# Performance work log

Hardware: AMD Instinct MI355X
Metric: run time of the kernel (lower is better)

Reference implementation:

```python
import jax, jax.numpy as jnp
import numpy as np

EPS = 1e-5
GROUPS = 32


def conv2d(x, w, b):
    # x: [N,C,H,W], w: [O,I,3,3] (or 1x1), stride 1, padding 'same' for 3x3
    kh = w.shape[2]
    pad = (kh - 1) // 2
    y = jax.lax.conv_general_dilated(x, w, (1, 1), ((pad, pad), (pad, pad)),
                                     dimension_numbers=('NCHW', 'OIHW', 'NCHW'))
    return y + b[None, :, None, None]


def group_norm(x, g, b):
    N, C, H, W = x.shape
    xr = x.reshape(N, GROUPS, C // GROUPS, H, W)
    mu = xr.mean(axis=(2, 3, 4), keepdims=True)
    var = xr.var(axis=(2, 3, 4), keepdims=True)
    xr = (xr - mu) / jnp.sqrt(var + EPS)
    return xr.reshape(N, C, H, W) * g[None, :, None, None] + b[None, :, None, None]


def batch_norm(x, g, b):
    # training-mode BatchNorm2d: batch statistics over (N,H,W)
    mu = x.mean(axis=(0, 2, 3), keepdims=True)
    var = x.var(axis=(0, 2, 3), keepdims=True)
    return (x - mu) / jnp.sqrt(var + EPS) * g[None, :, None, None] + b[None, :, None, None]


def binary_activation(x):
    # STE: forward sign(x), backward through piecewise poly out3
    out_fwd = jnp.sign(x)
    m1 = (x < -1).astype(x.dtype)
    m2 = (x < 0).astype(x.dtype)
    m3 = (x < 1).astype(x.dtype)
    out1 = -1.0 * m1 + (x * x + 2.0 * x) * (1.0 - m1)
    out2 = out1 * m2 + (-x * x + 2.0 * x) * (1.0 - m2)
    out3 = out2 * m3 + 1.0 * (1.0 - m3)
    return jax.lax.stop_gradient(out_fwd - out3) + out3


def hard_binary_conv(x, w, b):
    # per-output-channel scaling * sign(w), STE through clipped weights
    scale = jax.lax.stop_gradient(jnp.mean(jnp.abs(w), axis=(1, 2, 3), keepdims=True))
    bw_ng = scale * jnp.sign(w)
    clipped = jnp.clip(w, -1.0, 1.0)
    bw = jax.lax.stop_gradient(bw_ng - clipped) + clipped
    return conv2d(x, bw, b)


def learnable_bias(x, emb, w, b):
    bias = jax.nn.silu(emb) @ w.T + b  # [B, C]
    return x + bias[:, :, None, None]


def _forward(c, x, emb,
             rb_gn1_g, rb_gn1_b, rb_conv1_w, rb_conv1_b, rb_emb_w, rb_emb_b,
             rb_gn2_g, rb_gn2_b, rb_conv2_w, rb_conv2_b,
             m1_w, m1_b, bconv_w, bconv_b, bn_g, bn_b,
             m2_w, m2_b, prelu_a, m3_w, m3_b):
    # ResBlock (skip = Identity since out_channels == channels)
    h = conv2d(jax.nn.silu(group_norm(c, rb_gn1_g, rb_gn1_b)), rb_conv1_w, rb_conv1_b)
    eo = jax.nn.silu(emb) @ rb_emb_w.T + rb_emb_b          # [B, 2*C]
    scale, shift = jnp.split(eo[:, :, None, None], 2, axis=1)
    h = group_norm(h, rb_gn2_g, rb_gn2_b) * (1.0 + scale) + shift
    h = conv2d(jax.nn.silu(h), rb_conv2_w, rb_conv2_b)
    c2 = c + h
    # concat + bias + STE binarize + binary conv + BN + channel-pool residual + PReLU
    xc = jnp.concatenate([x, c2], axis=1)                   # [B, 2C, H, W]
    out = learnable_bias(xc, emb, m1_w, m1_b)
    out = binary_activation(out)
    out = hard_binary_conv(out, bconv_w, bconv_b)
    out = batch_norm(out, bn_g, bn_b)
    N, C2, H, W = xc.shape
    out = out + xc.reshape(N, C2 // 2, 2, H, W).mean(axis=2)  # channel mean pooling
    out = learnable_bias(out, emb, m2_w, m2_b)
    out = jnp.where(out >= 0, out, prelu_a[None, :, None, None] * out)  # PReLU
    out = learnable_bias(out, emb, m3_w, m3_b)
    return out


def setup_inputs() -> dict:
    key = jax.random.key(0)
    ks = jax.random.split(key, 24)
    B, C, EMB, H, W = 8, 128, 512, 64, 64
    IN2 = 2 * C
    n = lambda k, s, sc=0.05: jax.random.normal(k, s, dtype=jnp.float32) * sc
    return {
        'c': jax.random.normal(ks[0], (B, C, H, W), dtype=jnp.float32),
        'x': jax.random.normal(ks[1], (B, C, H, W), dtype=jnp.float32),
        'emb': jax.random.normal(ks[2], (B, EMB), dtype=jnp.float32),
        'rb_gn1_g': jnp.ones((C,), jnp.float32), 'rb_gn1_b': jnp.zeros((C,), jnp.float32),
        'rb_conv1_w': n(ks[3], (C, C, 3, 3)), 'rb_conv1_b': n(ks[4], (C,)),
        'rb_emb_w': n(ks[5], (2 * C, EMB)), 'rb_emb_b': n(ks[6], (2 * C,)),
        'rb_gn2_g': jnp.ones((C,), jnp.float32), 'rb_gn2_b': jnp.zeros((C,), jnp.float32),
        'rb_conv2_w': n(ks[7], (C, C, 3, 3)), 'rb_conv2_b': n(ks[8], (C,)),
        'm1_w': n(ks[9], (IN2, EMB)), 'm1_b': n(ks[10], (IN2,)),
        'bconv_w': jax.random.uniform(ks[11], (C, IN2, 3, 3), dtype=jnp.float32) * 0.001,
        'bconv_b': n(ks[12], (C,)),
        'bn_g': jnp.ones((C,), jnp.float32), 'bn_b': jnp.zeros((C,), jnp.float32),
        'm2_w': n(ks[13], (C, EMB)), 'm2_b': n(ks[14], (C,)),
        'prelu_a': jnp.full((C,), 0.25, jnp.float32),
        'm3_w': n(ks[15], (C, EMB)), 'm3_b': n(ks[16], (C,)),
    }


def reference(c, x, emb,
              rb_gn1_g, rb_gn1_b, rb_conv1_w, rb_conv1_b, rb_emb_w, rb_emb_b,
              rb_gn2_g, rb_gn2_b, rb_conv2_w, rb_conv2_b,
              m1_w, m1_b, bconv_w, bconv_b, bn_g, bn_b,
              m2_w, m2_b, prelu_a, m3_w, m3_b):
    return _forward(c, x, emb,
                    rb_gn1_g, rb_gn1_b, rb_conv1_w, rb_conv1_b, rb_emb_w, rb_emb_b,
                    rb_gn2_g, rb_gn2_b, rb_conv2_w, rb_conv2_b,
                    m1_w, m1_b, bconv_w, bconv_b, bn_g, bn_b,
                    m2_w, m2_b, prelu_a, m3_w, m3_b)
```

## Files before the change

### kernel.cpp

```cpp
#include <hip/hip_runtime.h>
#include <stdint.h>


#define B_   8
#define C_   128
#define C2_  256
#define HW_  4096
#define EMB_ 512
#define EPS_ 1e-5f

typedef int   v16i __attribute__((ext_vector_type(16)));
typedef float v16f __attribute__((ext_vector_type(16)));
typedef short v8s  __attribute__((ext_vector_type(8)));
typedef int   v4i  __attribute__((ext_vector_type(4)));

#define COLB 272
#define ROWB (66 * COLB)
#define LDSZ 55296
#define TSTRIDE 132

__device__ __forceinline__ float silu(float v) {
    return v * __builtin_amdgcn_rcpf(1.f + __expf(-v));
}
__device__ __forceinline__ unsigned short f2bf(float f) {
    unsigned int x = __float_as_uint(f);
    return (unsigned short)((x + 0x7FFFu + ((x >> 16) & 1u)) >> 16);
}
__device__ __forceinline__ int8_t sgn8(float v) {
    return (v > 0.f) ? (int8_t)1 : ((v < 0.f) ? (int8_t)(-1) : (int8_t)0);
}
__device__ __forceinline__ void gld16(char* ldst, const char* gsrc) {
    __builtin_amdgcn_global_load_lds((const unsigned int*)gsrc,
                                     (unsigned int*)ldst, 16, 0, 0);
}

__global__ __launch_bounds__(256) void k_prep(
    const float* __restrict__ w, int8_t* __restrict__ sgn,
    float* __restrict__ alpha, float* __restrict__ bnPS, float* __restrict__ bnPQ,
    float* __restrict__ gnS, float* __restrict__ gnQ,
    const float* __restrict__ w1, const float* __restrict__ w2,
    unsigned short* __restrict__ Wc1, unsigned short* __restrict__ Wc2,
    const float* __restrict__ emb,
    const float* __restrict__ ew, const float* __restrict__ ebb,
    const float* __restrict__ m1w, const float* __restrict__ m1b,
    const float* __restrict__ m2w, const float* __restrict__ m2b,
    const float* __restrict__ m3w, const float* __restrict__ m3b,
    float* __restrict__ eo, float* __restrict__ b1,
    float* __restrict__ b2, float* __restrict__ b3,
    const float* __restrict__ gin,
    float* __restrict__ g1S, float* __restrict__ g1Q,
    int8_t* __restrict__ S) {
    __shared__ float red[256];
    const int blk = blockIdx.x, tid = threadIdx.x;
    if (blk < 128) {
        const int o = blk;
        if (o == 0) {
            for (int i = tid; i < 1024; i += 256) { bnPS[i] = 0.f; bnPQ[i] = 0.f; }
        }
        if (o == 1) { gnS[tid] = 0.f; }
        if (o == 2) { gnQ[tid] = 0.f; }
        const float* wr = w + (size_t)o * (C2_ * 9);
        float s = 0.f;
        for (int i = tid; i < C2_ * 9; i += 256) s += fabsf(wr[i]);
        red[tid] = s;
        __syncthreads();
        for (int st = 128; st > 0; st >>= 1) {
            if (tid < st) red[tid] += red[tid + st];
            __syncthreads();
        }
        if (tid == 0) alpha[o] = red[0] / (float)(C2_ * 9);
        for (int kk = 0; kk < 9; ++kk) {
            float v = wr[tid * 9 + kk];
            sgn[((size_t)(kk * 16 + (tid >> 4)) * C_ + o) * 16 + (tid & 15)] = sgn8(v);
        }
    } else if (blk < 704) {
        int i = (blk - 128) * 256 + tid;
        int co = i / (C_ * 9);
        int rem = i - co * (C_ * 9);
        int ci = rem / 9, kk = rem - ci * 9;
        size_t d = ((size_t)(kk * 16 + (ci >> 3)) * C_ + co) * 8 + (ci & 7);
        Wc1[d] = f2bf(w1[i]);
        Wc2[d] = f2bf(w2[i]);
    } else if (blk < 896) {
        const int o = (blk - 704) * 4 + (tid >> 6);
        const int l = tid & 63;
        const float* wv;
        float bias;
        float* dst;
        int dstride;
        if (o < 256)      { wv = ew  + (size_t)o * EMB_;              bias = ebb[o];    dst = eo + o;  dstride = 256; }
        else if (o < 512) { int r = o - 256; wv = m1w + (size_t)r * EMB_; bias = m1b[r]; dst = b1 + r; dstride = 256; }
        else if (o < 640) { int r = o - 512; wv = m2w + (size_t)r * EMB_; bias = m2b[r]; dst = b2 + r; dstride = 128; }
        else              { int r = o - 640; wv = m3w + (size_t)r * EMB_; bias = m3b[r]; dst = b3 + r; dstride = 128; }
        const float4 wa = *(const float4*)(wv + 8 * l);
        const float4 wb = *(const float4*)(wv + 8 * l + 4);
#pragma unroll
        for (int b = 0; b < B_; ++b) {
            const float* s = emb + b * EMB_ + 8 * l;
            float4 sa = *(const float4*)(s);
            float4 sb = *(const float4*)(s + 4);
            float p = wa.x * silu(sa.x) + wa.y * silu(sa.y) + wa.z * silu(sa.z) + wa.w * silu(sa.w) +
                      wb.x * silu(sb.x) + wb.y * silu(sb.y) + wb.z * silu(sb.z) + wb.w * silu(sb.w);
#pragma unroll
            for (int off = 32; off > 0; off >>= 1) p += __shfl_down(p, off, 64);
            if (l == 0) dst[b * dstride] = bias + p;
        }
    } else if (blk < 1408) {
        const int idx = blk - 896;
        const int n = idx >> 6, rest = idx & 63, grp = rest >> 1, h = rest & 1;
        const size_t base = ((size_t)(n * C_ + grp * 4)) << 12;
        float sum = 0.f, sq = 0.f;
        const float4* in4 = (const float4*)(gin + base);
        for (int i = tid + h * 2048; i < (h + 1) * 2048; i += 256) {
            float4 v = in4[i];
            sum += v.x + v.y + v.z + v.w;
            sq += v.x * v.x + v.y * v.y + v.z * v.z + v.w * v.w;
        }
#pragma unroll
        for (int off = 32; off > 0; off >>= 1) {
            sum += __shfl_xor(sum, off, 64);
            sq  += __shfl_xor(sq, off, 64);
        }
        if ((tid & 63) == 0) { red[tid >> 6] = sum; red[8 + (tid >> 6)] = sq; }
        __syncthreads();
        if (tid == 0) {
            g1S[h * 256 + n * 32 + grp] = red[0] + red[1] + red[2] + red[3];
            g1Q[h * 256 + n * 32 + grp] = red[8] + red[9] + red[10] + red[11];
        }
    } else {
        const int u = blk - 1408;
        const int n = u >> 1;
        const int row = (u & 1) * 65;
        int4* base = (int4*)(S + (size_t)n * 66 * ROWB + (size_t)row * ROWB);
        const int4 z = make_int4(0, 0, 0, 0);
        for (int i = tid; i < ROWB / 16; i += 256) base[i] = z;
    }
}

__global__ __launch_bounds__(512, 4) void k_conv1(
    const float* __restrict__ cin,
    const unsigned short* __restrict__ Wc,
    const float* __restrict__ bias,
    const float* __restrict__ g1w, const float* __restrict__ g1b,
    const float* __restrict__ g1S, const float* __restrict__ g1Q,
    float* __restrict__ outN,
    float* __restrict__ gnS, float* __restrict__ gnQ) {
    __shared__ __align__(16) char lds[LDSZ];
    __shared__ float chA[128], chB[128];
    const int y = blockIdx.x;
    const int n = blockIdx.y;
    const int tid = threadIdx.x;

    if (tid < 128) {
        const int ch = tid, grp = tid >> 2;
        const float s1 = g1S[n * 32 + grp] + g1S[256 + n * 32 + grp];
        const float q1 = g1Q[n * 32 + grp] + g1Q[256 + n * 32 + grp];
        const float mu = s1 * (1.f / 16384.f);
        const float var = q1 * (1.f / 16384.f) - mu * mu;
        const float rstd = rsqrtf(var + EPS_);
        const float A = g1w[ch] * rstd;
        chA[ch] = A;
        chB[ch] = g1b[ch] - mu * A;
    }
    if (tid < 96) {
        int r = tid / 32, q = tid & 31;
        int c = (q >> 4) ? 65 : 0, o = q & 15;
        *(float4*)(lds + (r * 66 + c) * COLB + o * 16) = make_float4(0.f, 0.f, 0.f, 0.f);
    }
    __syncthreads();

    union F4 { float4 v; float f[4]; };
#pragma unroll
    for (int u = 0; u < 6; ++u) {
        int unit = u * 512 + tid;
        int r = unit >> 10, rem = unit & 1023;
        int cp = rem >> 4, s4 = rem & 15;
        int ch0 = 2 * cp;
        int yy = y - 1 + r;
        char* dst0 = lds + (r * 66 + 4 * s4 + 1) * COLB + 4 * cp;
        if (yy >= 0 && yy < 64) {
            const float* src = cin + (((size_t)(n * C_ + ch0)) << 12) + yy * 64 + 4 * s4;
            F4 fa, fb;
            fa.v = *(const float4*)src;
            fb.v = *(const float4*)(src + HW_);
            const float A0 = chA[ch0], B0 = chB[ch0];
            const float A1 = chA[ch0 + 1], B1 = chB[ch0 + 1];
#pragma unroll
            for (int e = 0; e < 4; ++e) {
                unsigned int lo = f2bf(silu(fa.f[e] * A0 + B0));
                unsigned int hi = f2bf(silu(fb.f[e] * A1 + B1));
                *(unsigned int*)(dst0 + e * COLB) = lo | (hi << 16);
            }
        } else {
#pragma unroll
            for (int e = 0; e < 4; ++e)
                *(unsigned int*)(dst0 + e * COLB) = 0u;
        }
    }
    __syncthreads();

    const int w = tid >> 6;
    const int og = w >> 1;
    const int ph = w & 1;
    const int l = tid & 63;
    const int lm = l & 31;
    const int lh = l >> 5;

    v16f acc;
#pragma unroll
    for (int i = 0; i < 16; ++i) acc[i] = 0.f;

#pragma unroll
    for (int kk = 0; kk < 9; ++kk) {
        const int r = kk / 3, dx = kk % 3 - 1;
        const char* col = lds + (r * 66 + 32 * ph + lm + 1 + dx) * COLB + 16 * lh;
        const unsigned short* wbase = Wc + (size_t)(kk * 16 + lh) * C_ * 8 + (32 * og + lm) * 8;
#pragma unroll
        for (int cb = 0; cb < 8; ++cb) {
            v8s a = *(const v8s*)(wbase + (size_t)(2 * cb) * C_ * 8);
            v8s b = *(const v8s*)(col + 32 * cb);
            acc = __builtin_amdgcn_mfma_f32_32x32x16_bf16(a, b, acc, 0, 0, 0);
        }
    }
    __syncthreads();
    float* ldsT = (float*)lds;
    float* ldsS = (float*)(lds + 64 * TSTRIDE * 4);
    float* ldsQ = ldsS + 256;
#pragma unroll
    for (int r = 0; r < 16; ++r) {
        const int row = (r & 3) + 8 * (r >> 2) + 4 * lh;
        const int co = 32 * og + row;
        float v = acc[r] + bias[co];
        ldsT[(32 * ph + lm) * TSTRIDE + co] = v;
        float p = v, q = v * v;
#pragma unroll
        for (int m = 16; m > 0; m >>= 1) {
            p += __shfl_xor(p, m, 64);
            q += __shfl_xor(q, m, 64);
        }
        if (lm == 0) { ldsS[ph * 128 + co] = p; ldsQ[ph * 128 + co] = q; }
    }
    __syncthreads();
    if (tid < 32) {
        const int g = tid;
        float p = 0.f, q = 0.f;
#pragma unroll
        for (int j = 0; j < 4; ++j) {
            p += ldsS[4 * g + j] + ldsS[128 + 4 * g + j];
            q += ldsQ[4 * g + j] + ldsQ[128 + 4 * g + j];
        }
        atomicAdd(&gnS[n * 32 + g], p);
        atomicAdd(&gnQ[n * 32 + g], q);
    }
    const int q4 = tid & 31;
    float* orow = outN + (((size_t)(n * HW_) + (y << 6)) << 7);
#pragma unroll
    for (int it = 0; it < 4; ++it) {
        const int px = it * 16 + (tid >> 5);
        *(float4*)(orow + ((size_t)px << 7) + 4 * q4) =
            *(const float4*)(ldsT + px * TSTRIDE + 4 * q4);
    }
}

__global__ __launch_bounds__(512, 4) void k_conv2(
    const float* __restrict__ yin,
    const unsigned short* __restrict__ Wc,
    const float* __restrict__ bias,
    const float* __restrict__ res,
    const float* __restrict__ xin,
    const float* __restrict__ b1v,
    const float* __restrict__ eo,
    const float* __restrict__ g2,
    const float* __restrict__ bt2,
    const float* __restrict__ gnS,
    const float* __restrict__ gnQ,
    float* __restrict__ poolC2,
    int8_t* __restrict__ S) {
    __shared__ __align__(16) char lds[LDSZ];
    __shared__ float ldsA[128], ldsB[128];
    const int y = blockIdx.x;
    const int n = blockIdx.y;
    const int tid = threadIdx.x;

    if (tid < 128) {
        const int ch = tid, grp = tid >> 2;
        const float mu = gnS[n * 32 + grp] * (1.f / 16384.f);
        const float var = gnQ[n * 32 + grp] * (1.f / 16384.f) - mu * mu;
        const float rstd = rsqrtf(var + EPS_);
        const float gg = g2[ch] * rstd;
        const float sc = 1.f + eo[n * 256 + ch];
        ldsA[ch] = gg * sc;
        ldsB[ch] = (bt2[ch] - mu * gg) * sc + eo[n * 256 + 128 + ch];
    }
    if (tid < 96) {
        int r = tid / 32, q = tid & 31;
        int cpad = (q >> 4) ? 65 : 0, o = q & 15;
        *(float4*)(lds + (r * 66 + cpad) * COLB + o * 16) = make_float4(0.f, 0.f, 0.f, 0.f);
    }
    __syncthreads();

    const int qc = tid & 31;
    const float A0 = ldsA[4 * qc], A1 = ldsA[4 * qc + 1], A2 = ldsA[4 * qc + 2], A3 = ldsA[4 * qc + 3];
    const float B0 = ldsB[4 * qc], B1 = ldsB[4 * qc + 1], B2 = ldsB[4 * qc + 2], B3 = ldsB[4 * qc + 3];
#pragma unroll
    for (int r = 0; r < 3; ++r) {
        const int yy = y - 1 + r;
        const float* ysrc = yin + (((size_t)(n * HW_) + yy * 64) << 7);
        const bool ok = (yy >= 0 && yy < 64);
#pragma unroll
        for (int it = 0; it < 4; ++it) {
            const int px = it * 16 + (tid >> 5);
            char* dst = lds + (r * 66 + px + 1) * COLB + qc * 8;
            if (ok) {
                float4 v = *(const float4*)(ysrc + ((size_t)px << 7) + 4 * qc);
                union { unsigned short u[4]; uint2 q; } pk;
                pk.u[0] = f2bf(silu(v.x * A0 + B0));
                pk.u[1] = f2bf(silu(v.y * A1 + B1));
                pk.u[2] = f2bf(silu(v.z * A2 + B2));
                pk.u[3] = f2bf(silu(v.w * A3 + B3));
                *(uint2*)dst = pk.q;
            } else {
                *(uint2*)dst = make_uint2(0u, 0u);
            }
        }
    }
    __syncthreads();

    const int w = tid >> 6;
    const int og = w >> 1;
    const int ph = w & 1;
    const int l = tid & 63;
    const int lm = l & 31;
    const int lh = l >> 5;

    v16f acc;
#pragma unroll
    for (int i = 0; i < 16; ++i) acc[i] = 0.f;

#pragma unroll
    for (int kk = 0; kk < 9; ++kk) {
        const int r = kk / 3, dx = kk % 3 - 1;
        const char* col = lds + (r * 66 + 32 * ph + lm + 1 + dx) * COLB + 16 * lh;
        const unsigned short* wbase = Wc + (size_t)(kk * 16 + lh) * C_ * 8 + (32 * og + lm) * 8;
#pragma unroll
        for (int cb = 0; cb < 8; ++cb) {
            v8s a = *(const v8s*)(wbase + (size_t)(2 * cb) * C_ * 8);
            v8s b = *(const v8s*)(col + 32 * cb);
            acc = __builtin_amdgcn_mfma_f32_32x32x16_bf16(a, b, acc, 0, 0, 0);
        }
    }
    float c2v[16];
#pragma unroll
    for (int r = 0; r < 16; ++r) {
        const int row = (r & 3) + 8 * (r >> 2) + 4 * lh;
        const int co = 32 * og + row;
        const size_t o = (((size_t)n * C_ + co) << 12) + (y << 6);
        c2v[r] = acc[r] + bias[co] + res[o + 32 * ph + lm];
    }
#pragma unroll
    for (int q = 0; q < 4; ++q) {
        const int pc = 16 * og + 4 * q + 2 * lh;
        const size_t po = (((size_t)n * 64 + pc) << 12) + (y << 6);
        poolC2[po + 32 * ph + lm]        = 0.5f * (c2v[4 * q] + c2v[4 * q + 1]);
        poolC2[po + 4096 + 32 * ph + lm] = 0.5f * (c2v[4 * q + 2] + c2v[4 * q + 3]);
    }

    __syncthreads();
#pragma unroll
    for (int q = 0; q < 4; ++q) {
        const int co0 = 32 * og + 8 * q + 4 * lh;
        const float b0 = b1v[n * 256 + 128 + co0];
        const float b1b = b1v[n * 256 + 128 + co0 + 1];
        const float b2b = b1v[n * 256 + 128 + co0 + 2];
        const float b3b = b1v[n * 256 + 128 + co0 + 3];
        union { int8_t b[4]; int u; } p0;
        p0.b[0] = sgn8(c2v[4 * q] + b0);
        p0.b[1] = sgn8(c2v[4 * q + 1] + b1b);
        p0.b[2] = sgn8(c2v[4 * q + 2] + b2b);
        p0.b[3] = sgn8(c2v[4 * q + 3] + b3b);
        *(int*)(lds + (32 * ph + lm + 1) * COLB + 128 + co0) = p0.u;
    }
#pragma unroll
    for (int u = 0; u < 4; ++u) {
        int idx = u * 512 + tid;
        int ch = idx >> 4, seg = idx & 15;
        float4 v = *(const float4*)(xin + (((size_t)(n * C_ + ch)) << 12) + (y << 6) + 4 * seg);
        const float bv = b1v[n * 256 + ch];
        lds[(4 * seg + 1) * COLB + ch] = sgn8(v.x + bv);
        lds[(4 * seg + 2) * COLB + ch] = sgn8(v.y + bv);
        lds[(4 * seg + 3) * COLB + ch] = sgn8(v.z + bv);
        lds[(4 * seg + 4) * COLB + ch] = sgn8(v.w + bv);
    }
    if (tid < 34) {
        int c = tid / 17, o = tid - c * 17;
        *(float4*)(lds + (c ? 65 : 0) * COLB + o * 16) = make_float4(0.f, 0.f, 0.f, 0.f);
    }
    __syncthreads();
    int4* Srow = (int4*)(S + (size_t)n * 66 * ROWB + (size_t)(y + 1) * ROWB);
    const int4* lsrc = (const int4*)lds;
    for (int i = tid; i < ROWB / 16; i += 512) Srow[i] = lsrc[i];
}

__global__ __launch_bounds__(512, 2) void k_bconv(
    const int8_t* __restrict__ S,
    const int8_t* __restrict__ Wk,
    const float* __restrict__ alpha,
    const float* __restrict__ bias,
    float* __restrict__ out,
    float* __restrict__ bnPS, float* __restrict__ bnPQ) {
    __shared__ __align__(16) char lds[LDSZ];
    const int y = blockIdx.x;
    const int n = blockIdx.y;
    const int tid = threadIdx.x;
    const char* src3 = (const char*)S + (size_t)n * 66 * ROWB + (size_t)y * ROWB;
    const int wave = tid >> 6, lane = tid & 63;
    for (int u = wave; u < 53; u += 8)
        gld16(lds + u * 1024, src3 + u * 1024 + lane * 16);
    __syncthreads();

    const int w = tid >> 6;
    const int og = w >> 1;
    const int ph = w & 1;
    const int l = tid & 63;
    const int lm = l & 31;
    const int lh = l >> 5;

    v16i acc;
#pragma unroll
    for (int i = 0; i < 16; ++i) acc[i] = 0;

#pragma unroll
    for (int kk = 0; kk < 9; ++kk) {
        const int r = kk / 3, dx = kk % 3 - 1;
        const char* col = lds + (r * 66 + 32 * ph + lm + 1 + dx) * COLB + 16 * lh;
        const int8_t* wbase = Wk + (size_t)(kk * 16 + lh) * C_ * 16 + (32 * og + lm) * 16;
#pragma unroll
        for (int s = 0; s < 8; ++s) {
            v4i a = *(const v4i*)(wbase + (size_t)(2 * s) * C_ * 16);
            v4i b = *(const v4i*)(col + 32 * s);
            acc = __builtin_amdgcn_mfma_i32_32x32x32_i8(a, b, acc, 0, 0, 0);
        }
    }
    __syncthreads();
    float* ldsS = (float*)lds;
    float* ldsQ = (float*)lds + 256;
#pragma unroll
    for (int r = 0; r < 16; ++r) {
        const int row = (r & 3) + 8 * (r >> 2) + 4 * lh;
        const int co = 32 * og + row;
        const float av = alpha[co], bv = bias[co];
        const size_t o = (((size_t)n * C_ + co) << 12) + (y << 6);
        float v = av * (float)acc[r] + bv;
        out[o + 32 * ph + lm] = v;
        float p = v, q = v * v;
#pragma unroll
        for (int m = 16; m > 0; m >>= 1) {
            p += __shfl_xor(p, m, 64);
            q += __shfl_xor(q, m, 64);
        }
        if (lm == 0) { ldsS[ph * 128 + co] = p; ldsQ[ph * 128 + co] = q; }
    }
    __syncthreads();
    if (tid < 128) {
        atomicAdd(&bnPS[n * 128 + tid], ldsS[tid] + ldsS[128 + tid]);
        atomicAdd(&bnPQ[n * 128 + tid], ldsQ[tid] + ldsQ[128 + tid]);
    }
}

__global__ __launch_bounds__(256) void k_final(const float* __restrict__ y3,
                                               const float* __restrict__ x,
                                               const float* __restrict__ poolC2,
                                               const float* __restrict__ bnPS,
                                               const float* __restrict__ bnPQ,
                                               const float* __restrict__ bng,
                                               const float* __restrict__ bnb,
                                               const float* __restrict__ b2v,
                                               const float* __restrict__ pa,
                                               const float* __restrict__ b3v,
                                               float* __restrict__ out) {
    const int idx4 = blockIdx.x * 256 + threadIdx.x;
    const int hw = (idx4 & 1023) * 4;
    const int cb = idx4 >> 10;
    const int co = cb & 127;
    const int n = cb >> 7;
    float sS = 0.f, sQ = 0.f;
#pragma unroll
    for (int j = 0; j < 8; ++j) { sS += bnPS[j * 128 + co]; sQ += bnPQ[j * 128 + co]; }
    const float mu = sS * (1.f / 32768.f);
    const float var = sQ * (1.f / 32768.f) - mu * mu;
    const float rstd = rsqrtf(var + EPS_);
    const float gm = rstd * bng[co];
    const float bt = bnb[co] - mu * gm;
    const size_t obase = (((size_t)(n * C_ + co)) << 12) + hw;
    float4 v = *(const float4*)(y3 + obase);
    v.x = v.x * gm + bt; v.y = v.y * gm + bt; v.z = v.z * gm + bt; v.w = v.w * gm + bt;

    float4 pv;
    if (co < 64) {
        const int ch0 = 2 * co;
        float4 pA = *(const float4*)(x + (((size_t)(n * C_ + ch0)) << 12) + hw);
        float4 pB = *(const float4*)(x + (((size_t)(n * C_ + ch0 + 1)) << 12) + hw);
        pv.x = 0.5f * (pA.x + pB.x); pv.y = 0.5f * (pA.y + pB.y);
        pv.z = 0.5f * (pA.z + pB.z); pv.w = 0.5f * (pA.w + pB.w);
    } else {
        pv = *(const float4*)(poolC2 + (((size_t)(n * 64 + co - 64)) << 12) + hw);
    }
    const float bias2 = b2v[n * 128 + co];
    const float aP = pa[co];
    const float bias3 = b3v[n * 128 + co];
    float4 r;
    float t;
    t = v.x + pv.x + bias2; t = (t >= 0.f) ? t : aP * t; r.x = t + bias3;
    t = v.y + pv.y + bias2; t = (t >= 0.f) ? t : aP * t; r.y = t + bias3;
    t = v.z + pv.z + bias2; t = (t >= 0.f) ? t : aP * t; r.z = t + bias3;
    t = v.w + pv.w + bias2; t = (t >= 0.f) ? t : aP * t; r.w = t + bias3;
    *(float4*)(out + obase) = r;
}

extern "C" void kernel_launch(void* const* d_in, const int* in_sizes, int n_in,
                              void* d_out, int out_size, void* d_ws, size_t ws_size,
                              hipStream_t stream) {
    const float* c       = (const float*)d_in[0];
    const float* x       = (const float*)d_in[1];
    const float* emb     = (const float*)d_in[2];
    const float* gn1_g   = (const float*)d_in[3];
    const float* gn1_b   = (const float*)d_in[4];
    const float* conv1_w = (const float*)d_in[5];
    const float* conv1_b = (const float*)d_in[6];
    const float* emb_w   = (const float*)d_in[7];
    const float* emb_b   = (const float*)d_in[8];
    const float* gn2_g   = (const float*)d_in[9];
    const float* gn2_b   = (const float*)d_in[10];
    const float* conv2_w = (const float*)d_in[11];
    const float* conv2_b = (const float*)d_in[12];
    const float* m1_w    = (const float*)d_in[13];
    const float* m1_b    = (const float*)d_in[14];
    const float* bconv_w = (const float*)d_in[15];
    const float* bconv_b = (const float*)d_in[16];
    const float* bn_g    = (const float*)d_in[17];
    const float* bn_b    = (const float*)d_in[18];
    const float* m2_w    = (const float*)d_in[19];
    const float* m2_b    = (const float*)d_in[20];
    const float* prelu_a = (const float*)d_in[21];
    const float* m3_w    = (const float*)d_in[22];
    const float* m3_b    = (const float*)d_in[23];
    float* out = (float*)d_out;

    float* ws = (float*)d_ws;
    const size_t NCHW = (size_t)B_ * C_ * HW_;
    float*  poolC2 = ws;
    float*  y_buf = ws + NCHW;
    int8_t* S     = (int8_t*)(ws + 2 * NCHW);
    const size_t S_f = (8 * 66 * (size_t)ROWB) / 4 + 512;
    int8_t* sgn   = (int8_t*)(ws + 2 * NCHW + S_f);
    unsigned short* Wc1 = (unsigned short*)(ws + 2 * NCHW + S_f + 73728);
    unsigned short* Wc2 = Wc1 + C_ * C_ * 9;
    float*  alpha = ws + 2 * NCHW + S_f + 73728 + 2 * 73728;
    float*  eo    = alpha + 128;
    float*  b1v   = eo + B_ * 256;
    float*  b2v   = b1v + B_ * 256;
    float*  b3v   = b2v + B_ * 128;
    float*  bnPS  = b3v + B_ * 128;
    float*  bnPQ  = bnPS + 1024;
    float*  gnS   = bnPQ + 1024;
    float*  gnQ   = gnS + 256;
    float*  g1S   = gnQ + 256;
    float*  g1Q   = g1S + 512;

    k_prep<<<1424, 256, 0, stream>>>(bconv_w, sgn, alpha, bnPS, bnPQ, gnS, gnQ,
                                     conv1_w, conv2_w, Wc1, Wc2,
                                     emb, emb_w, emb_b, m1_w, m1_b, m2_w, m2_b,
                                     m3_w, m3_b, eo, b1v, b2v, b3v,
                                     c, g1S, g1Q, S);
    k_conv1<<<dim3(64, B_), 512, 0, stream>>>(c, Wc1, conv1_b, gn1_g, gn1_b,
                                              g1S, g1Q, y_buf, gnS, gnQ);
    k_conv2<<<dim3(64, B_), 512, 0, stream>>>(y_buf, Wc2, conv2_b, c, x, b1v, eo,
                                              gn2_g, gn2_b, gnS, gnQ, poolC2, S);
    k_bconv<<<dim3(64, B_), 512, 0, stream>>>(S, sgn, alpha, bconv_b, y_buf,
                                              bnPS, bnPQ);
    k_final<<<NCHW / 1024, 256, 0, stream>>>(y_buf, x, poolC2, bnPS, bnPQ,
                                             bn_g, bn_b, b2v, prelu_a, b3v, out);
}
```

Baseline: 208.9 us.

## Shrink LDS footprint and raise occupancy bounds in conv kernels

Cuts the shared-memory arrays in the conv1, conv2 and bconv kernels to the exact tile sizes and drops the per-channel scale/shift LDS tables. Each thread now computes its own group-norm affine coefficients in registers, which removes one barrier per block. Launch bounds are raised to 6 blocks per CU so more blocks fit per CU and latency is better hidden. The cost is redundant global reads for the coefficients and tighter register budgets, which could cause spills.

```diff
diff --git a/kernel.cpp b/kernel.cpp
--- a/kernel.cpp
+++ b/kernel.cpp
@@ -16,7 +16,8 @@
 
 #define COLB 272
 #define ROWB (66 * COLB)
-#define LDSZ 55296
+#define TILEB (3 * ROWB)
+#define BLDS (53 * 1024)
 #define TSTRIDE 132
 
 __device__ __forceinline__ float silu(float v) {
@@ -137,7 +138,7 @@
     }
 }
 
-__global__ __launch_bounds__(512, 4) void k_conv1(
+__global__ __launch_bounds__(512, 6) void k_conv1(
     const float* __restrict__ cin,
     const unsigned short* __restrict__ Wc,
     const float* __restrict__ bias,
@@ -145,46 +146,52 @@
     const float* __restrict__ g1S, const float* __restrict__ g1Q,
     float* __restrict__ outN,
     float* __restrict__ gnS, float* __restrict__ gnQ) {
-    __shared__ __align__(16) char lds[LDSZ];
-    __shared__ float chA[128], chB[128];
+    __shared__ __align__(16) char lds[TILEB];
     const int y = blockIdx.x;
     const int n = blockIdx.y;
     const int tid = threadIdx.x;
 
-    if (tid < 128) {
-        const int ch = tid, grp = tid >> 2;
-        const float s1 = g1S[n * 32 + grp] + g1S[256 + n * 32 + grp];
-        const float q1 = g1Q[n * 32 + grp] + g1Q[256 + n * 32 + grp];
-        const float mu = s1 * (1.f / 16384.f);
-        const float var = q1 * (1.f / 16384.f) - mu * mu;
-        const float rstd = rsqrtf(var + EPS_);
-        const float A = g1w[ch] * rstd;
-        chA[ch] = A;
-        chB[ch] = g1b[ch] - mu * A;
+    const int t4 = tid >> 4;
+    const int s4 = tid & 15;
+    float Ae0, Be0, Ae1, Be1, Ao0, Bo0, Ao1, Bo1;
+    {
+        const int g0 = t4 >> 1;
+        float s1 = g1S[n * 32 + g0] + g1S[256 + n * 32 + g0];
+        float q1 = g1Q[n * 32 + g0] + g1Q[256 + n * 32 + g0];
+        float mu = s1 * (1.f / 16384.f);
+        float rstd = rsqrtf(q1 * (1.f / 16384.f) - mu * mu + EPS_);
+        Ae0 = g1w[2 * t4] * rstd;     Be0 = g1b[2 * t4] - mu * Ae0;
+        Ae1 = g1w[2 * t4 + 1] * rstd; Be1 = g1b[2 * t4 + 1] - mu * Ae1;
+        const int g1i = 16 + (t4 >> 1);
+        s1 = g1S[n * 32 + g1i] + g1S[256 + n * 32 + g1i];
+        q1 = g1Q[n * 32 + g1i] + g1Q[256 + n * 32 + g1i];
+        mu = s1 * (1.f / 16384.f);
+        rstd = rsqrtf(q1 * (1.f / 16384.f) - mu * mu + EPS_);
+        Ao0 = g1w[64 + 2 * t4] * rstd; Bo0 = g1b[64 + 2 * t4] - mu * Ao0;
+        Ao1 = g1w[65 + 2 * t4] * rstd; Bo1 = g1b[65 + 2 * t4] - mu * Ao1;
     }
     if (tid < 96) {
         int r = tid / 32, q = tid & 31;
         int c = (q >> 4) ? 65 : 0, o = q & 15;
         *(float4*)(lds + (r * 66 + c) * COLB + o * 16) = make_float4(0.f, 0.f, 0.f, 0.f);
     }
-    __syncthreads();
 
     union F4 { float4 v; float f[4]; };
 #pragma unroll
     for (int u = 0; u < 6; ++u) {
-        int unit = u * 512 + tid;
-        int r = unit >> 10, rem = unit & 1023;
-        int cp = rem >> 4, s4 = rem & 15;
-        int ch0 = 2 * cp;
-        int yy = y - 1 + r;
+        const int r = u >> 1;
+        const int odd = u & 1;
+        const int cp = (odd ? 32 : 0) + t4;
+        const int ch0 = 2 * cp;
+        const int yy = y - 1 + r;
         char* dst0 = lds + (r * 66 + 4 * s4 + 1) * COLB + 4 * cp;
         if (yy >= 0 && yy < 64) {
             const float* src = cin + (((size_t)(n * C_ + ch0)) << 12) + yy * 64 + 4 * s4;
             F4 fa, fb;
             fa.v = *(const float4*)src;
             fb.v = *(const float4*)(src + HW_);
-            const float A0 = chA[ch0], B0 = chB[ch0];
-            const float A1 = chA[ch0 + 1], B1 = chB[ch0 + 1];
+            const float A0 = odd ? Ao0 : Ae0, B0 = odd ? Bo0 : Be0;
+            const float A1 = odd ? Ao1 : Ae1, B1 = odd ? Bo1 : Be1;
 #pragma unroll
             for (int e = 0; e < 4; ++e) {
                 unsigned int lo = f2bf(silu(fa.f[e] * A0 + B0));
@@ -262,7 +269,7 @@
     }
 }
 
-__global__ __launch_bounds__(512, 4) void k_conv2(
+__global__ __launch_bounds__(512, 6) void k_conv2(
     const float* __restrict__ yin,
     const unsigned short* __restrict__ Wc,
     const float* __restrict__ bias,
@@ -276,32 +283,34 @@
     const float* __restrict__ gnQ,
     float* __restrict__ poolC2,
     int8_t* __restrict__ S) {
-    __shared__ __align__(16) char lds[LDSZ];
-    __shared__ float ldsA[128], ldsB[128];
+    __shared__ __align__(16) char lds[TILEB];
     const int y = blockIdx.x;
     const int n = blockIdx.y;
     const int tid = threadIdx.x;
 
-    if (tid < 128) {
-        const int ch = tid, grp = tid >> 2;
-        const float mu = gnS[n * 32 + grp] * (1.f / 16384.f);
-        const float var = gnQ[n * 32 + grp] * (1.f / 16384.f) - mu * mu;
+    const int qc = tid & 31;
+    float A0, A1, A2, A3, B0, B1, B2, B3;
+    {
+        const float mu = gnS[n * 32 + qc] * (1.f / 16384.f);
+        const float var = gnQ[n * 32 + qc] * (1.f / 16384.f) - mu * mu;
         const float rstd = rsqrtf(var + EPS_);
-        const float gg = g2[ch] * rstd;
-        const float sc = 1.f + eo[n * 256 + ch];
-        ldsA[ch] = gg * sc;
-        ldsB[ch] = (bt2[ch] - mu * gg) * sc + eo[n * 256 + 128 + ch];
+        const int ch = 4 * qc;
+        float gg, sc;
+        gg = g2[ch] * rstd;     sc = 1.f + eo[n * 256 + ch];
+        A0 = gg * sc; B0 = (bt2[ch] - mu * gg) * sc + eo[n * 256 + 128 + ch];
+        gg = g2[ch + 1] * rstd; sc = 1.f + eo[n * 256 + ch + 1];
+        A1 = gg * sc; B1 = (bt2[ch + 1] - mu * gg) * sc + eo[n * 256 + 128 + ch + 1];
+        gg = g2[ch + 2] * rstd; sc = 1.f + eo[n * 256 + ch + 2];
+        A2 = gg * sc; B2 = (bt2[ch + 2] - mu * gg) * sc + eo[n * 256 + 128 + ch + 2];
+        gg = g2[ch + 3] * rstd; sc = 1.f + eo[n * 256 + ch + 3];
+        A3 = gg * sc; B3 = (bt2[ch + 3] - mu * gg) * sc + eo[n * 256 + 128 + ch + 3];
     }
     if (tid < 96) {
         int r = tid / 32, q = tid & 31;
         int cpad = (q >> 4) ? 65 : 0, o = q & 15;
         *(float4*)(lds + (r * 66 + cpad) * COLB + o * 16) = make_float4(0.f, 0.f, 0.f, 0.f);
     }
-    __syncthreads();
-
-    const int qc = tid & 31;
-    const float A0 = ldsA[4 * qc], A1 = ldsA[4 * qc + 1], A2 = ldsA[4 * qc + 2], A3 = ldsA[4 * qc + 3];
-    const float B0 = ldsB[4 * qc], B1 = ldsB[4 * qc + 1], B2 = ldsB[4 * qc + 2], B3 = ldsB[4 * qc + 3];
+
 #pragma unroll
     for (int r = 0; r < 3; ++r) {
         const int yy = y - 1 + r;
@@ -401,14 +410,14 @@
     for (int i = tid; i < ROWB / 16; i += 512) Srow[i] = lsrc[i];
 }
 
-__global__ __launch_bounds__(512, 2) void k_bconv(
+__global__ __launch_bounds__(512, 6) void k_bconv(
     const int8_t* __restrict__ S,
     const int8_t* __restrict__ Wk,
     const float* __restrict__ alpha,
     const float* __restrict__ bias,
     float* __restrict__ out,
     float* __restrict__ bnPS, float* __restrict__ bnPQ) {
-    __shared__ __align__(16) char lds[LDSZ];
+    __shared__ __align__(16) char lds[BLDS];
     const int y = blockIdx.x;
     const int n = blockIdx.y;
     const int tid = threadIdx.x;
```

After: 211.1 us. About the same (+1.1%).

## Move conv2/bconv weight prep and embedding GEMVs into conv1 as extra blocks

Applied to the files above, without the earlier changes.

Prep work not needed by conv1 (binary weight sign/alpha, conv2 weight bf16 packing, embedding projections) moves out of k_prep and runs as extra blocks appended to the k_conv1 grid. This shortens the serial prep kernel ahead of conv1 and lets that work overlap with the conv1 tiles. k_conv1's grid becomes 1D with 1024 blocks, and the zeroing of the reduction buffers moves into a dedicated prep block. The extra blocks use 512 threads and may delay conv1 tiles or add register pressure to the fused kernel.

```diff
diff --git a/kernel.cpp b/kernel.cpp
--- a/kernel.cpp
+++ b/kernel.cpp
@@ -35,78 +35,23 @@
 }
 
 __global__ __launch_bounds__(256) void k_prep(
-    const float* __restrict__ w, int8_t* __restrict__ sgn,
-    float* __restrict__ alpha, float* __restrict__ bnPS, float* __restrict__ bnPQ,
-    float* __restrict__ gnS, float* __restrict__ gnQ,
-    const float* __restrict__ w1, const float* __restrict__ w2,
-    unsigned short* __restrict__ Wc1, unsigned short* __restrict__ Wc2,
-    const float* __restrict__ emb,
-    const float* __restrict__ ew, const float* __restrict__ ebb,
-    const float* __restrict__ m1w, const float* __restrict__ m1b,
-    const float* __restrict__ m2w, const float* __restrict__ m2b,
-    const float* __restrict__ m3w, const float* __restrict__ m3b,
-    float* __restrict__ eo, float* __restrict__ b1,
-    float* __restrict__ b2, float* __restrict__ b3,
+    const float* __restrict__ w1, unsigned short* __restrict__ Wc1,
     const float* __restrict__ gin,
     float* __restrict__ g1S, float* __restrict__ g1Q,
-    int8_t* __restrict__ S) {
+    int8_t* __restrict__ S,
+    float* __restrict__ bnPS, float* __restrict__ bnPQ,
+    float* __restrict__ gnS, float* __restrict__ gnQ) {
     __shared__ float red[256];
     const int blk = blockIdx.x, tid = threadIdx.x;
-    if (blk < 128) {
-        const int o = blk;
-        if (o == 0) {
-            for (int i = tid; i < 1024; i += 256) { bnPS[i] = 0.f; bnPQ[i] = 0.f; }
-        }
-        if (o == 1) { gnS[tid] = 0.f; }
-        if (o == 2) { gnQ[tid] = 0.f; }
-        const float* wr = w + (size_t)o * (C2_ * 9);
-        float s = 0.f;
-        for (int i = tid; i < C2_ * 9; i += 256) s += fabsf(wr[i]);
-        red[tid] = s;
-        __syncthreads();
-        for (int st = 128; st > 0; st >>= 1) {
-            if (tid < st) red[tid] += red[tid + st];
-            __syncthreads();
-        }
-        if (tid == 0) alpha[o] = red[0] / (float)(C2_ * 9);
-        for (int kk = 0; kk < 9; ++kk) {
-            float v = wr[tid * 9 + kk];
-            sgn[((size_t)(kk * 16 + (tid >> 4)) * C_ + o) * 16 + (tid & 15)] = sgn8(v);
-        }
-    } else if (blk < 704) {
-        int i = (blk - 128) * 256 + tid;
+    if (blk < 576) {
+        int i = blk * 256 + tid;
         int co = i / (C_ * 9);
         int rem = i - co * (C_ * 9);
         int ci = rem / 9, kk = rem - ci * 9;
         size_t d = ((size_t)(kk * 16 + (ci >> 3)) * C_ + co) * 8 + (ci & 7);
         Wc1[d] = f2bf(w1[i]);
-        Wc2[d] = f2bf(w2[i]);
-    } else if (blk < 896) {
-        const int o = (blk - 704) * 4 + (tid >> 6);
-        const int l = tid & 63;
-        const float* wv;
-        float bias;
-        float* dst;
-        int dstride;
-        if (o < 256)      { wv = ew  + (size_t)o * EMB_;              bias = ebb[o];    dst = eo + o;  dstride = 256; }
-        else if (o < 512) { int r = o - 256; wv = m1w + (size_t)r * EMB_; bias = m1b[r]; dst = b1 + r; dstride = 256; }
-        else if (o < 640) { int r = o - 512; wv = m2w + (size_t)r * EMB_; bias = m2b[r]; dst = b2 + r; dstride = 128; }
-        else              { int r = o - 640; wv = m3w + (size_t)r * EMB_; bias = m3b[r]; dst = b3 + r; dstride = 128; }
-        const float4 wa = *(const float4*)(wv + 8 * l);
-        const float4 wb = *(const float4*)(wv + 8 * l + 4);
-#pragma unroll
-        for (int b = 0; b < B_; ++b) {
-            const float* s = emb + b * EMB_ + 8 * l;
-            float4 sa = *(const float4*)(s);
-            float4 sb = *(const float4*)(s + 4);
-            float p = wa.x * silu(sa.x) + wa.y * silu(sa.y) + wa.z * silu(sa.z) + wa.w * silu(sa.w) +
-                      wb.x * silu(sb.x) + wb.y * silu(sb.y) + wb.z * silu(sb.z) + wb.w * silu(sb.w);
-#pragma unroll
-            for (int off = 32; off > 0; off >>= 1) p += __shfl_down(p, off, 64);
-            if (l == 0) dst[b * dstride] = bias + p;
-        }
-    } else if (blk < 1408) {
-        const int idx = blk - 896;
+    } else if (blk < 1088) {
+        const int idx = blk - 576;
         const int n = idx >> 6, rest = idx & 63, grp = rest >> 1, h = rest & 1;
         const size_t base = ((size_t)(n * C_ + grp * 4)) << 12;
         float sum = 0.f, sq = 0.f;
@@ -127,13 +72,17 @@
             g1S[h * 256 + n * 32 + grp] = red[0] + red[1] + red[2] + red[3];
             g1Q[h * 256 + n * 32 + grp] = red[8] + red[9] + red[10] + red[11];
         }
-    } else {
-        const int u = blk - 1408;
+    } else if (blk < 1104) {
+        const int u = blk - 1088;
         const int n = u >> 1;
         const int row = (u & 1) * 65;
         int4* base = (int4*)(S + (size_t)n * 66 * ROWB + (size_t)row * ROWB);
         const int4 z = make_int4(0, 0, 0, 0);
         for (int i = tid; i < ROWB / 16; i += 256) base[i] = z;
+    } else {
+        for (int i = tid; i < 1024; i += 256) { bnPS[i] = 0.f; bnPQ[i] = 0.f; }
+        gnS[tid] = 0.f;
+        gnQ[tid] = 0.f;
     }
 }
 
@@ -144,12 +93,80 @@
     const float* __restrict__ g1w, const float* __restrict__ g1b,
     const float* __restrict__ g1S, const float* __restrict__ g1Q,
     float* __restrict__ outN,
-    float* __restrict__ gnS, float* __restrict__ gnQ) {
+    float* __restrict__ gnS, float* __restrict__ gnQ,
+    const float* __restrict__ wq, int8_t* __restrict__ sgn,
+    float* __restrict__ alpha,
+    const float* __restrict__ w2, unsigned short* __restrict__ Wc2,
+    const float* __restrict__ emb,
+    const float* __restrict__ ew, const float* __restrict__ ebb,
+    const float* __restrict__ m1w, const float* __restrict__ m1b,
+    const float* __restrict__ m2w, const float* __restrict__ m2b,
+    const float* __restrict__ m3w, const float* __restrict__ m3b,
+    float* __restrict__ eo, float* __restrict__ b1,
+    float* __restrict__ b2, float* __restrict__ b3) {
     __shared__ __align__(16) char lds[LDSZ];
     __shared__ float chA[128], chB[128];
-    const int y = blockIdx.x;
-    const int n = blockIdx.y;
+    const int blk = blockIdx.x;
     const int tid = threadIdx.x;
+
+    if (blk >= 512) {
+        if (blk < 640) {
+            float* red = (float*)lds;
+            const int o = blk - 512;
+            const float* wr = wq + (size_t)o * (C2_ * 9);
+            float s = 0.f;
+            for (int i = tid; i < C2_ * 9; i += 512) s += fabsf(wr[i]);
+            red[tid] = s;
+            __syncthreads();
+            for (int st = 256; st > 0; st >>= 1) {
+                if (tid < st) red[tid] += red[tid + st];
+                __syncthreads();
+            }
+            if (tid == 0) alpha[o] = red[0] / (float)(C2_ * 9);
+            if (tid < 256) {
+#pragma unroll
+                for (int kk = 0; kk < 9; ++kk) {
+                    float v = wr[tid * 9 + kk];
+                    sgn[((size_t)(kk * 16 + (tid >> 4)) * C_ + o) * 16 + (tid & 15)] = sgn8(v);
+                }
+            }
+        } else if (blk < 928) {
+            int i = (blk - 640) * 512 + tid;
+            int co = i / (C_ * 9);
+            int rem = i - co * (C_ * 9);
+            int ci = rem / 9, kk = rem - ci * 9;
+            size_t d = ((size_t)(kk * 16 + (ci >> 3)) * C_ + co) * 8 + (ci & 7);
+            Wc2[d] = f2bf(w2[i]);
+        } else {
+            const int o = (blk - 928) * 8 + (tid >> 6);
+            const int l = tid & 63;
+            const float* wv;
+            float bv;
+            float* dst;
+            int dstride;
+            if (o < 256)      { wv = ew  + (size_t)o * EMB_;              bv = ebb[o];    dst = eo + o;  dstride = 256; }
+            else if (o < 512) { int r = o - 256; wv = m1w + (size_t)r * EMB_; bv = m1b[r]; dst = b1 + r; dstride = 256; }
+            else if (o < 640) { int r = o - 512; wv = m2w + (size_t)r * EMB_; bv = m2b[r]; dst = b2 + r; dstride = 128; }
+            else              { int r = o - 640; wv = m3w + (size_t)r * EMB_; bv = m3b[r]; dst = b3 + r; dstride = 128; }
+            const float4 wa = *(const float4*)(wv + 8 * l);
+            const float4 wb = *(const float4*)(wv + 8 * l + 4);
+#pragma unroll
+            for (int b = 0; b < B_; ++b) {
+                const float* s = emb + b * EMB_ + 8 * l;
+                float4 sa = *(const float4*)(s);
+                float4 sb = *(const float4*)(s + 4);
+                float p = wa.x * silu(sa.x) + wa.y * silu(sa.y) + wa.z * silu(sa.z) + wa.w * silu(sa.w) +
+                          wb.x * silu(sb.x) + wb.y * silu(sb.y) + wb.z * silu(sb.z) + wb.w * silu(sb.w);
+#pragma unroll
+                for (int off = 32; off > 0; off >>= 1) p += __shfl_down(p, off, 64);
+                if (l == 0) dst[b * dstride] = bv + p;
+            }
+        }
+        return;
+    }
+
+    const int y = blk & 63;
+    const int n = blk >> 6;
 
     if (tid < 128) {
         const int ch = tid, grp = tid >> 2;
@@ -567,13 +584,14 @@
     float*  g1S   = gnQ + 256;
     float*  g1Q   = g1S + 512;
 
-    k_prep<<<1424, 256, 0, stream>>>(bconv_w, sgn, alpha, bnPS, bnPQ, gnS, gnQ,
-                                     conv1_w, conv2_w, Wc1, Wc2,
-                                     emb, emb_w, emb_b, m1_w, m1_b, m2_w, m2_b,
-                                     m3_w, m3_b, eo, b1v, b2v, b3v,
-                                     c, g1S, g1Q, S);
-    k_conv1<<<dim3(64, B_), 512, 0, stream>>>(c, Wc1, conv1_b, gn1_g, gn1_b,
-                                              g1S, g1Q, y_buf, gnS, gnQ);
+    k_prep<<<1105, 256, 0, stream>>>(conv1_w, Wc1, c, g1S, g1Q, S,
+                                     bnPS, bnPQ, gnS, gnQ);
+    k_conv1<<<1024, 512, 0, stream>>>(c, Wc1, conv1_b, gn1_g, gn1_b,
+                                      g1S, g1Q, y_buf, gnS, gnQ,
+                                      bconv_w, sgn, alpha, conv2_w, Wc2,
+                                      emb, emb_w, emb_b, m1_w, m1_b,
+                                      m2_w, m2_b, m3_w, m3_b,
+                                      eo, b1v, b2v, b3v);
     k_conv2<<<dim3(64, B_), 512, 0, stream>>>(y_buf, Wc2, conv2_b, c, x, b1v, eo,
                                               gn2_g, gn2_b, gnS, gnQ, poolC2, S);
     k_bconv<<<dim3(64, B_), 512, 0, stream>>>(S, sgn, alpha, bconv_b, y_buf,
```

Result: no change. 208.4 us (-0.2%).
